# Kernel optimization log

Hardware: AMD Instinct MI355X
Metric: run time of the kernel (lower is better)

Reference implementation:

```python
import jax, jax.numpy as jnp
import numpy as np

N_HEADS = 16
EPS = 1e-5  # torch nn.LayerNorm default


def layernorm(x, g, b):
    mu = x.mean(-1, keepdims=True)
    var = ((x - mu) ** 2).mean(-1, keepdims=True)
    return (x - mu) * jax.lax.rsqrt(var + EPS) * g + b


def setup_inputs() -> dict:
    V, D, Dff, L, S, B = 32000, 1024, 4096, 6, 2048, 1
    key = jax.random.key(0)
    ks = jax.random.split(key, 12)
    std = 0.02  # GPT-2 init
    nrm = lambda k, shp: jax.random.normal(k, shp, jnp.float32) * std
    return {
        "tokens": jax.random.randint(ks[0], (B, S), 0, V),
        "tok_emb": nrm(ks[1], (V, D)),          # tied with lm head
        "pos_emb": nrm(ks[2], (S, D)),
        "Wq": nrm(ks[3], (L, D, D)), "bq": jnp.zeros((L, D)),
        "Wk": nrm(ks[4], (L, D, D)), "bk": jnp.zeros((L, D)),
        "Wv": nrm(ks[5], (L, D, D)), "bv": jnp.zeros((L, D)),
        "Wo": nrm(ks[6], (L, D, D)), "bo": jnp.zeros((L, D)),
        "ln1_g": jnp.ones((L, D)), "ln1_b": jnp.zeros((L, D)),
        "ln2_g": jnp.ones((L, D)), "ln2_b": jnp.zeros((L, D)),
        "W1": nrm(ks[7], (L, D, Dff)), "b1": jnp.zeros((L, Dff)),
        "W2": nrm(ks[8], (L, Dff, D)), "b2": jnp.zeros((L, D)),
        "lnf_g": jnp.ones((D,)), "lnf_b": jnp.zeros((D,)),
    }


def reference(tokens, tok_emb, pos_emb, Wq, bq, Wk, bk, Wv, bv, Wo, bo,
              ln1_g, ln1_b, ln2_g, ln2_b, W1, b1, W2, b2, lnf_g, lnf_b):
    B, S = tokens.shape
    D = tok_emb.shape[1]
    dk = D // N_HEADS
    scale = 1.0 / np.sqrt(dk)

    x = tok_emb[tokens] + pos_emb[:S][None]           # (B,S,D); dropout p=0 -> identity
    causal = jnp.tril(jnp.ones((S, S), bool))

    def block(x, p):
        wq, bq_, wk, bk_, wv, bv_, wo, bo_, g1, b1_, g2, b2_, w1, bf1, w2, bf2 = p
        # --- attention sublayer (pre-norm) ---
        h = layernorm(x, g1, b1_)
        q = (h @ wq + bq_).reshape(B, S, N_HEADS, dk)
        k = (h @ wk + bk_).reshape(B, S, N_HEADS, dk)
        v = (h @ wv + bv_).reshape(B, S, N_HEADS, dk)
        scores = jnp.einsum('bqhd,bkhd->bhqk', q, k) * scale
        scores = jnp.where(causal, scores, -jnp.inf)   # masked_fill(mask==0, -inf)
        attn = jax.nn.softmax(scores, axis=-1)
        ctx = jnp.einsum('bhqk,bkhd->bqhd', attn, v).reshape(B, S, D)
        x = x + ctx @ wo + bo_
        # --- FFN sublayer (pre-norm) ---
        h = layernorm(x, g2, b2_)
        x = x + jax.nn.gelu(h @ w1 + bf1, approximate=False) @ w2 + bf2
        return x, None

    x, _ = jax.lax.scan(
        block, x,
        (Wq, bq, Wk, bk, Wv, bv, Wo, bo, ln1_g, ln1_b, ln2_g, ln2_b, W1, b1, W2, b2))
    x = layernorm(x, lnf_g, lnf_b)
    logits = x @ tok_emb.T                             # tied lm head (no bias)
    return logits
```

## Files before the change

### kernel.cpp

```cpp
#include <hip/hip_runtime.h>
#include <hip/hip_bf16.h>
#include <cstdint>
#include <cstddef>


typedef __attribute__((ext_vector_type(4))) float  f32x4;
typedef __attribute__((ext_vector_type(8))) __bf16 bf16x8;
typedef __attribute__((ext_vector_type(4))) __bf16 bf16x4;

#define S_LEN 2048
#define DMODEL 1024
#define DFF 4096
#define NLAYER 6
#define NHEAD 16
#define DK 64
#define VOCAB 32000

__device__ __forceinline__ void gload_lds16(const void* g, void* l) {
    __builtin_amdgcn_global_load_lds(
        (__attribute__((address_space(1))) void*)(void*)(g),
        (__attribute__((address_space(3))) void*)(l), 16, 0, 0);
}

__global__ __launch_bounds__(256) void transpose_cvt64(
    const float* __restrict__ in, __bf16* __restrict__ out,
    int K, int N, size_t in_lstride, size_t out_lstride) {
    __shared__ float tile[64][65];
    const float* inp = in + blockIdx.z * in_lstride;
    __bf16* outp = out + blockIdx.z * out_lstride;
    const int n0 = blockIdx.x * 64, k0 = blockIdx.y * 64;
    const int t = threadIdx.x;
    const int lc = t & 15, rr = t >> 4;
#pragma unroll
    for (int i = 0; i < 4; ++i) {
        float4 v = *(const float4*)&inp[(size_t)(k0 + rr + i * 16) * N + n0 + lc * 4];
        tile[rr + i * 16][lc * 4 + 0] = v.x;
        tile[rr + i * 16][lc * 4 + 1] = v.y;
        tile[rr + i * 16][lc * 4 + 2] = v.z;
        tile[rr + i * 16][lc * 4 + 3] = v.w;
    }
    __syncthreads();
    const int a = t & 7, b = t >> 3;
#pragma unroll
    for (int j = 0; j < 2; ++j) {
        const int n = b + j * 32;
        bf16x8 o;
#pragma unroll
        for (int e = 0; e < 8; ++e) o[e] = (__bf16)tile[a * 8 + e][n];
        *(bf16x8*)&outp[(size_t)(n0 + n) * K + k0 + a * 8] = o;
    }
}

__global__ __launch_bounds__(256) void cvt_bf16(
    const float* __restrict__ in, __bf16* __restrict__ out, long n4) {
    long i = (long)blockIdx.x * 256 + threadIdx.x;
    if (i >= n4) return;
    float4 v = ((const float4*)in)[i];
    bf16x4 o = {(__bf16)v.x, (__bf16)v.y, (__bf16)v.z, (__bf16)v.w};
    ((bf16x4*)out)[i] = o;
}

__global__ __launch_bounds__(256) void embed_kernel(
    const int* __restrict__ tokens, const float* __restrict__ te,
    const float* __restrict__ pe, float* __restrict__ x) {
    const int s = blockIdx.x, t = threadIdx.x;
    const int tok = tokens[s];
    float4 a = ((const float4*)(te + (size_t)tok * DMODEL))[t];
    float4 p = ((const float4*)(pe + (size_t)s * DMODEL))[t];
    float4 r = {a.x + p.x, a.y + p.y, a.z + p.z, a.w + p.w};
    ((float4*)(x + (size_t)s * DMODEL))[t] = r;
}

__global__ __launch_bounds__(256) void ln_kernel(
    const float* __restrict__ x, const float* __restrict__ g,
    const float* __restrict__ b, __bf16* __restrict__ out) {
    const int row = blockIdx.x, t = threadIdx.x;
    float4 v = ((const float4*)(x + (size_t)row * DMODEL))[t];
    float s  = v.x + v.y + v.z + v.w;
    float s2 = v.x * v.x + v.y * v.y + v.z * v.z + v.w * v.w;
#pragma unroll
    for (int off = 1; off < 64; off <<= 1) {
        s  += __shfl_xor(s, off);
        s2 += __shfl_xor(s2, off);
    }
    __shared__ float ss[4], ss2[4];
    const int wave = t >> 6;
    if ((t & 63) == 0) { ss[wave] = s; ss2[wave] = s2; }
    __syncthreads();
    s  = ss[0] + ss[1] + ss[2] + ss[3];
    s2 = ss2[0] + ss2[1] + ss2[2] + ss2[3];
    const float mu  = s * (1.0f / DMODEL);
    const float var = s2 * (1.0f / DMODEL) - mu * mu;
    const float rstd = rsqrtf(var + 1e-5f);
    float4 gg = ((const float4*)g)[t];
    float4 bb = ((const float4*)b)[t];
    __bf16* o = out + (size_t)row * DMODEL + t * 4;
    o[0] = (__bf16)((v.x - mu) * rstd * gg.x + bb.x);
    o[1] = (__bf16)((v.y - mu) * rstd * gg.y + bb.y);
    o[2] = (__bf16)((v.z - mu) * rstd * gg.z + bb.z);
    o[3] = (__bf16)((v.w - mu) * rstd * gg.w + bb.w);
}

template <int BM, int BN, int BK, int SPLITK, int MODE, int XCD>
__global__ __launch_bounds__(256) void gemm_tiled(
    const __bf16* __restrict__ A, const __bf16* __restrict__ BT,
    int M, int N, int K,
    const float* __restrict__ bias,
    float* __restrict__ fout,
    __bf16* __restrict__ bfout,
    __bf16* __restrict__ qb, __bf16* __restrict__ kb, __bf16* __restrict__ vb,
    const float* __restrict__ bq, const float* __restrict__ bk,
    const float* __restrict__ bv) {
    constexpr int SLOTS = BK / 8;
    constexpr int SH    = (BK == 64) ? 0 : 1;
    constexpr int RPC   = 2048 / BK;
    constexpr int ACH_A = BM / RPC;
    constexpr int ACH_B = BN / RPC;
    constexpr int LOADS = ACH_A + ACH_B;
    constexpr int MR = BM / 32;
    constexpr int NR = BN / 32;
    constexpr int KS = BK / 32;
    __shared__ alignas(16) __bf16 As[2][BM * BK];
    __shared__ alignas(16) __bf16 Bs[2][BN * BK];
    const int t = threadIdx.x;
    const int wave = t >> 6, lane = t & 63;
    const int wr = wave >> 1, wc = wave & 1;
    const int lg = lane >> 4, lr = lane & 15;

    int bx = blockIdx.x, by = blockIdx.y;
    if (XCD) {
        const int nwg = gridDim.x * gridDim.y;
        const int wgid = by * gridDim.x + bx;
        const int sw = (wgid & 7) * (nwg >> 3) + (wgid >> 3);
        bx = sw % gridDim.x;
        by = sw / gridDim.x;
    }
    const int row0 = bx * BM, col0 = by * BN;
    const int kz = (SPLITK > 1) ? blockIdx.z : 0;
    const int Ksl = K / SPLITK;

    f32x4 acc[MR][NR];
#pragma unroll
    for (int i = 0; i < MR; i++)
#pragma unroll
        for (int j = 0; j < NR; j++) acc[i][j] = f32x4{0.f, 0.f, 0.f, 0.f};

    const int srow = t / SLOTS;
    const int sks = ((t % SLOTS) ^ ((srow >> SH) & (SLOTS - 1))) * 8;
    const __bf16* Ab = A + (size_t)(row0 + srow) * K + kz * Ksl + sks;
    const __bf16* Bb = BT + (size_t)(col0 + srow) * K + kz * Ksl + sks;

    const int nt = Ksl / BK;
#pragma unroll
    for (int ch = 0; ch < ACH_A; ++ch)
        gload_lds16(Ab + (size_t)ch * RPC * K, &As[0][ch * 2048 + wave * 512]);
#pragma unroll
    for (int ch = 0; ch < ACH_B; ++ch)
        gload_lds16(Bb + (size_t)ch * RPC * K, &Bs[0][ch * 2048 + wave * 512]);

    int c = 0;
    for (int T = 0; T < nt; ++T) {
        if (T + 1 < nt) {
            const int k0 = (T + 1) * BK;
#pragma unroll
            for (int ch = 0; ch < ACH_A; ++ch)
                gload_lds16(Ab + (size_t)ch * RPC * K + k0,
                            &As[c ^ 1][ch * 2048 + wave * 512]);
#pragma unroll
            for (int ch = 0; ch < ACH_B; ++ch)
                gload_lds16(Bb + (size_t)ch * RPC * K + k0,
                            &Bs[c ^ 1][ch * 2048 + wave * 512]);
            if constexpr (LOADS == 3)
                asm volatile("s_waitcnt vmcnt(3)" ::: "memory");
            else if constexpr (LOADS == 4)
                asm volatile("s_waitcnt vmcnt(4)" ::: "memory");
            else if constexpr (LOADS == 6)
                asm volatile("s_waitcnt vmcnt(6)" ::: "memory");
            else
                asm volatile("s_waitcnt vmcnt(8)" ::: "memory");
        } else {
            asm volatile("s_waitcnt vmcnt(0)" ::: "memory");
        }
        __builtin_amdgcn_s_barrier();
        asm volatile("" ::: "memory");

        bf16x8 af[MR][KS], bfr[NR][KS];
#pragma unroll
        for (int i = 0; i < MR; i++)
#pragma unroll
            for (int ks = 0; ks < KS; ks++) {
                const int row = wr * (BM / 2) + i * 16 + lr;
                const int ph = ((ks * 4 + lg) ^ ((row >> SH) & (SLOTS - 1)));
                af[i][ks] = *(const bf16x8*)&As[c][row * BK + ph * 8];
            }
#pragma unroll
        for (int j = 0; j < NR; j++)
#pragma unroll
            for (int ks = 0; ks < KS; ks++) {
                const int n = wc * (BN / 2) + j * 16 + lr;
                const int ph = ((ks * 4 + lg) ^ ((n >> SH) & (SLOTS - 1)));
                bfr[j][ks] = *(const bf16x8*)&Bs[c][n * BK + ph * 8];
            }
        __builtin_amdgcn_s_setprio(1);
#pragma unroll
        for (int i = 0; i < MR; i++)
#pragma unroll
            for (int j = 0; j < NR; j++)
#pragma unroll
                for (int ks = 0; ks < KS; ks++)
                    acc[i][j] = __builtin_amdgcn_mfma_f32_16x16x32_bf16(
                        af[i][ks], bfr[j][ks], acc[i][j], 0, 0, 0);
        __builtin_amdgcn_s_setprio(0);
        asm volatile("" ::: "memory");
        __builtin_amdgcn_s_barrier();
        c ^= 1;
    }

#pragma unroll
    for (int i = 0; i < MR; i++) {
#pragma unroll
        for (int j = 0; j < NR; j++) {
#pragma unroll
            for (int r = 0; r < 4; r++) {
                const int row = row0 + wr * (BM / 2) + i * 16 + lg * 4 + r;
                const int col = col0 + wc * (BN / 2) + j * 16 + lr;
                float v = acc[i][j][r];
                if (MODE == 0) {
                    const int sec = col >> 10, cn = col & 1023;
                    const int head = cn >> 6, d = cn & 63;
                    if (sec == 0) {
                        v = (v + bq[cn]) * 0.125f;
                        qb[((size_t)head * S_LEN + row) * DK + d] = (__bf16)v;
                    } else if (sec == 1) {
                        v = v + bk[cn];
                        kb[((size_t)head * S_LEN + row) * DK + d] = (__bf16)v;
                    } else {
                        v = v + bv[cn];
                        vb[((size_t)head * DK + d) * S_LEN + row] = (__bf16)v;
                    }
                } else if (MODE == 1) {
                    const size_t idx = (size_t)row * N + col;
                    if (SPLITK > 1) {
                        atomicAdd(&fout[idx], v + (kz == 0 ? bias[col] : 0.f));
                    } else {
                        fout[idx] = fout[idx] + v + bias[col];
                    }
                } else if (MODE == 2) {
                    const float gg = v + bias[col];
                    const float cgl = 0.5f * gg * (1.0f + erff(gg * 0.70710678118654752f));
                    bfout[(size_t)row * N + col] = (__bf16)cgl;
                } else {
                    __builtin_nontemporal_store(v, &fout[(size_t)row * N + col]);
                }
            }
        }
    }
}

__global__ __launch_bounds__(256) void attn_kernel(
    const __bf16* __restrict__ q, const __bf16* __restrict__ k,
    const __bf16* __restrict__ vt, __bf16* __restrict__ ctx) {
    const int qblk = blockIdx.x, head = blockIdx.y;
    const int t = threadIdx.x;
    const int wave = t >> 6, lane = t & 63;
    const int lg = lane >> 4, lr = lane & 15;
    const int rowbase = qblk * 64 + wave * 16;

    const __bf16* qh = q + (size_t)head * S_LEN * DK;
    const __bf16* kh = k + (size_t)head * S_LEN * DK;
    const __bf16* vh = vt + (size_t)head * DK * S_LEN;

    __shared__ alignas(16) __bf16 pls[4][16 * 72];
    __bf16* pw = pls[wave];

    bf16x8 qf0 = *(const bf16x8*)&qh[(size_t)(rowbase + lr) * DK + lg * 8];
    bf16x8 qf1 = *(const bf16x8*)&qh[(size_t)(rowbase + lr) * DK + 32 + lg * 8];

    f32x4 oacc[4];
#pragma unroll
    for (int j = 0; j < 4; j++) oacc[j] = f32x4{0.f, 0.f, 0.f, 0.f};
    float m[4], l[4];
#pragma unroll
    for (int r = 0; r < 4; r++) { m[r] = -__builtin_inff(); l[r] = 0.f; }

    for (int tt = 0; tt <= qblk; ++tt) {
        const int kv0 = tt * 64;
        f32x4 sc[4];
        __builtin_amdgcn_s_setprio(1);
#pragma unroll
        for (int jn = 0; jn < 4; jn++) {
            bf16x8 kf0 = *(const bf16x8*)&kh[(size_t)(kv0 + jn * 16 + lr) * DK + lg * 8];
            bf16x8 kf1 = *(const bf16x8*)&kh[(size_t)(kv0 + jn * 16 + lr) * DK + 32 + lg * 8];
            sc[jn] = __builtin_amdgcn_mfma_f32_16x16x32_bf16(
                qf0, kf0, f32x4{0.f, 0.f, 0.f, 0.f}, 0, 0, 0);
            sc[jn] = __builtin_amdgcn_mfma_f32_16x16x32_bf16(qf1, kf1, sc[jn], 0, 0, 0);
        }
        __builtin_amdgcn_s_setprio(0);

        if (tt == qblk) {
#pragma unroll
            for (int jn = 0; jn < 4; jn++)
#pragma unroll
                for (int r = 0; r < 4; r++) {
                    const int qrow = rowbase + lg * 4 + r;
                    if (kv0 + jn * 16 + lr > qrow) sc[jn][r] = -__builtin_inff();
                }
        }

        float mt[4];
#pragma unroll
        for (int r = 0; r < 4; r++)
            mt[r] = fmaxf(fmaxf(sc[0][r], sc[1][r]), fmaxf(sc[2][r], sc[3][r]));
#pragma unroll
        for (int off = 1; off < 16; off <<= 1)
#pragma unroll
            for (int r = 0; r < 4; r++) mt[r] = fmaxf(mt[r], __shfl_xor(mt[r], off));

        float alpha[4], psum[4];
#pragma unroll
        for (int r = 0; r < 4; r++) {
            const float mn = fmaxf(m[r], mt[r]);
            alpha[r] = __expf(m[r] - mn);
            m[r] = mn;
#pragma unroll
            for (int jn = 0; jn < 4; jn++) sc[jn][r] = __expf(sc[jn][r] - mn);
            psum[r] = (sc[0][r] + sc[1][r]) + (sc[2][r] + sc[3][r]);
        }
#pragma unroll
        for (int off = 1; off < 16; off <<= 1)
#pragma unroll
            for (int r = 0; r < 4; r++) psum[r] += __shfl_xor(psum[r], off);
#pragma unroll
        for (int r = 0; r < 4; r++) l[r] = l[r] * alpha[r] + psum[r];
#pragma unroll
        for (int j = 0; j < 4; j++)
#pragma unroll
            for (int r = 0; r < 4; r++) oacc[j][r] *= alpha[r];

#pragma unroll
        for (int r = 0; r < 4; r++)
#pragma unroll
            for (int jn = 0; jn < 4; jn++)
                pw[(lg * 4 + r) * 72 + jn * 16 + lr] = (__bf16)sc[jn][r];

        bf16x8 pf0 = *(const bf16x8*)&pw[lr * 72 + lg * 8];
        bf16x8 pf1 = *(const bf16x8*)&pw[lr * 72 + 32 + lg * 8];
        __builtin_amdgcn_s_setprio(1);
#pragma unroll
        for (int j = 0; j < 4; j++) {
            bf16x8 vf0 = *(const bf16x8*)&vh[(size_t)(j * 16 + lr) * S_LEN + kv0 + lg * 8];
            oacc[j] = __builtin_amdgcn_mfma_f32_16x16x32_bf16(pf0, vf0, oacc[j], 0, 0, 0);
            bf16x8 vf1 = *(const bf16x8*)&vh[(size_t)(j * 16 + lr) * S_LEN + kv0 + 32 + lg * 8];
            oacc[j] = __builtin_amdgcn_mfma_f32_16x16x32_bf16(pf1, vf1, oacc[j], 0, 0, 0);
        }
        __builtin_amdgcn_s_setprio(0);
    }

#pragma unroll
    for (int j = 0; j < 4; j++)
#pragma unroll
        for (int r = 0; r < 4; r++) {
            const int row = rowbase + lg * 4 + r;
            ctx[(size_t)row * DMODEL + head * DK + j * 16 + lr] =
                (__bf16)(oacc[j][r] / l[r]);
        }
}

extern "C" void kernel_launch(void* const* d_in, const int* in_sizes, int n_in,
                              void* d_out, int out_size, void* d_ws, size_t ws_size,
                              hipStream_t stream) {
    const int*   tokens  = (const int*)d_in[0];
    const float* tok_emb = (const float*)d_in[1];
    const float* pos_emb = (const float*)d_in[2];
    const float* Wq = (const float*)d_in[3];
    const float* bq = (const float*)d_in[4];
    const float* Wk = (const float*)d_in[5];
    const float* bk = (const float*)d_in[6];
    const float* Wv = (const float*)d_in[7];
    const float* bv = (const float*)d_in[8];
    const float* Wo = (const float*)d_in[9];
    const float* bo = (const float*)d_in[10];
    const float* ln1_g = (const float*)d_in[11];
    const float* ln1_b = (const float*)d_in[12];
    const float* ln2_g = (const float*)d_in[13];
    const float* ln2_b = (const float*)d_in[14];
    const float* W1 = (const float*)d_in[15];
    const float* b1 = (const float*)d_in[16];
    const float* W2 = (const float*)d_in[17];
    const float* b2 = (const float*)d_in[18];
    const float* lnf_g = (const float*)d_in[19];
    const float* lnf_b = (const float*)d_in[20];

    char* ws = (char*)d_ws;
    size_t off = 0;
    auto alloc = [&](size_t bytes) {
        char* p = ws + off;
        off = (off + bytes + 255) & ~(size_t)255;
        return p;
    };
    __bf16* wqkv_t = (__bf16*)alloc((size_t)NLAYER * 3072 * 1024 * 2);
    __bf16* wo_t   = (__bf16*)alloc((size_t)NLAYER * 1024 * 1024 * 2);
    __bf16* w1_t   = (__bf16*)alloc((size_t)NLAYER * 4096 * 1024 * 2);
    __bf16* w2_t   = (__bf16*)alloc((size_t)NLAYER * 1024 * 4096 * 2);
    __bf16* temb   = (__bf16*)alloc((size_t)VOCAB * DMODEL * 2);
    float*  x      = (float*)alloc((size_t)S_LEN * DMODEL * 4);
    __bf16* h      = (__bf16*)alloc((size_t)S_LEN * DMODEL * 2);
    __bf16* qbuf   = (__bf16*)alloc((size_t)NHEAD * S_LEN * DK * 2);
    __bf16* kbuf   = (__bf16*)alloc((size_t)NHEAD * S_LEN * DK * 2);
    __bf16* vbuf   = (__bf16*)alloc((size_t)NHEAD * S_LEN * DK * 2);
    __bf16* ctx    = (__bf16*)alloc((size_t)S_LEN * DMODEL * 2);
    __bf16* ffn    = (__bf16*)alloc((size_t)S_LEN * DFF * 2);
    if (off > ws_size) return;

    const dim3 blk256(256);

    transpose_cvt64<<<dim3(16, 16, NLAYER), blk256, 0, stream>>>(
        Wq, wqkv_t + (size_t)0 * 1024 * 1024, 1024, 1024,
        (size_t)1024 * 1024, (size_t)3072 * 1024);
    transpose_cvt64<<<dim3(16, 16, NLAYER), blk256, 0, stream>>>(
        Wk, wqkv_t + (size_t)1 * 1024 * 1024, 1024, 1024,
        (size_t)1024 * 1024, (size_t)3072 * 1024);
    transpose_cvt64<<<dim3(16, 16, NLAYER), blk256, 0, stream>>>(
        Wv, wqkv_t + (size_t)2 * 1024 * 1024, 1024, 1024,
        (size_t)1024 * 1024, (size_t)3072 * 1024);
    transpose_cvt64<<<dim3(16, 16, NLAYER), blk256, 0, stream>>>(
        Wo, wo_t, 1024, 1024, (size_t)1024 * 1024, (size_t)1024 * 1024);
    transpose_cvt64<<<dim3(64, 16, NLAYER), blk256, 0, stream>>>(
        W1, w1_t, 1024, 4096, (size_t)1024 * 4096, (size_t)4096 * 1024);
    transpose_cvt64<<<dim3(16, 64, NLAYER), blk256, 0, stream>>>(
        W2, w2_t, 4096, 1024, (size_t)4096 * 1024, (size_t)1024 * 4096);
    cvt_bf16<<<dim3((VOCAB * DMODEL / 4 + 255) / 256), blk256, 0, stream>>>(
        tok_emb, temb, (long)VOCAB * DMODEL / 4);

    embed_kernel<<<dim3(S_LEN), blk256, 0, stream>>>(tokens, tok_emb, pos_emb, x);

    for (int l = 0; l < NLAYER; ++l) {
        ln_kernel<<<dim3(S_LEN), blk256, 0, stream>>>(
            x, ln1_g + l * 1024, ln1_b + l * 1024, h);
        gemm_tiled<64, 128, 64, 1, 0, 0><<<dim3(32, 24), blk256, 0, stream>>>(
            h, wqkv_t + (size_t)l * 3072 * 1024, S_LEN, 3072, 1024,
            nullptr, nullptr, nullptr, qbuf, kbuf, vbuf,
            bq + l * 1024, bk + l * 1024, bv + l * 1024);
        attn_kernel<<<dim3(S_LEN / 64, NHEAD), blk256, 0, stream>>>(
            qbuf, kbuf, vbuf, ctx);
        gemm_tiled<64, 128, 64, 2, 1, 0><<<dim3(32, 8, 2), blk256, 0, stream>>>(
            ctx, wo_t + (size_t)l * 1024 * 1024, S_LEN, 1024, 1024,
            bo + l * 1024, x, nullptr, nullptr, nullptr, nullptr,
            nullptr, nullptr, nullptr);
        ln_kernel<<<dim3(S_LEN), blk256, 0, stream>>>(
            x, ln2_g + l * 1024, ln2_b + l * 1024, h);
        gemm_tiled<128, 128, 64, 1, 2, 0><<<dim3(16, 32), blk256, 0, stream>>>(
            h, w1_t + (size_t)l * 4096 * 1024, S_LEN, 4096, 1024,
            b1 + l * 4096, nullptr, ffn, nullptr, nullptr, nullptr,
            nullptr, nullptr, nullptr);
        gemm_tiled<64, 128, 64, 2, 1, 0><<<dim3(32, 8, 2), blk256, 0, stream>>>(
            ffn, w2_t + (size_t)l * 1024 * 4096, S_LEN, 1024, 4096,
            b2 + l * 1024, x, nullptr, nullptr, nullptr, nullptr,
            nullptr, nullptr, nullptr);
    }

    ln_kernel<<<dim3(S_LEN), blk256, 0, stream>>>(x, lnf_g, lnf_b, h);
    gemm_tiled<128, 256, 32, 1, 3, 1><<<dim3(16, 125), blk256, 0, stream>>>(
        h, temb, S_LEN, VOCAB, 1024,
        nullptr, (float*)d_out, nullptr, nullptr, nullptr, nullptr,
        nullptr, nullptr, nullptr);
}
```

Before: 1.867 ms.

## Triple-buffer GEMM loads, replace split-K atomics with partials fused into layernorm

```diff
diff --git a/kernel.cpp b/kernel.cpp
--- a/kernel.cpp
+++ b/kernel.cpp
@@ -15,6 +15,7 @@
 #define NHEAD 16
 #define DK 64
 #define VOCAB 32000
+#define MN (S_LEN * DMODEL)
 
 __device__ __forceinline__ void gload_lds16(const void* g, void* l) {
     __builtin_amdgcn_global_load_lds(
@@ -71,11 +72,22 @@
     ((float4*)(x + (size_t)s * DMODEL))[t] = r;
 }
 
+template <int NPART>
 __global__ __launch_bounds__(256) void ln_kernel(
-    const float* __restrict__ x, const float* __restrict__ g,
-    const float* __restrict__ b, __bf16* __restrict__ out) {
+    float* __restrict__ x, const float* __restrict__ p,
+    const float* __restrict__ g, const float* __restrict__ b,
+    __bf16* __restrict__ out) {
     const int row = blockIdx.x, t = threadIdx.x;
     float4 v = ((const float4*)(x + (size_t)row * DMODEL))[t];
+    if (NPART == 2) {
+        float4 a0 = ((const float4*)(p + (size_t)row * DMODEL))[t];
+        float4 a1 = ((const float4*)(p + MN + (size_t)row * DMODEL))[t];
+        v.x += a0.x + a1.x;
+        v.y += a0.y + a1.y;
+        v.z += a0.z + a1.z;
+        v.w += a0.w + a1.w;
+        ((float4*)(x + (size_t)row * DMODEL))[t] = v;
+    }
     float s  = v.x + v.y + v.z + v.w;
     float s2 = v.x * v.x + v.y * v.y + v.z * v.z + v.w * v.w;
 #pragma unroll
@@ -120,8 +132,8 @@
     constexpr int MR = BM / 32;
     constexpr int NR = BN / 32;
     constexpr int KS = BK / 32;
-    __shared__ alignas(16) __bf16 As[2][BM * BK];
-    __shared__ alignas(16) __bf16 Bs[2][BN * BK];
+    __shared__ alignas(16) __bf16 As[3][BM * BK];
+    __shared__ alignas(16) __bf16 Bs[3][BN * BK];
     const int t = threadIdx.x;
     const int wave = t >> 6, lane = t & 63;
     const int wr = wave >> 1, wc = wave & 1;
@@ -151,38 +163,36 @@
     const __bf16* Bb = BT + (size_t)(col0 + srow) * K + kz * Ksl + sks;
 
     const int nt = Ksl / BK;
-#pragma unroll
-    for (int ch = 0; ch < ACH_A; ++ch)
-        gload_lds16(Ab + (size_t)ch * RPC * K, &As[0][ch * 2048 + wave * 512]);
-#pragma unroll
-    for (int ch = 0; ch < ACH_B; ++ch)
-        gload_lds16(Bb + (size_t)ch * RPC * K, &Bs[0][ch * 2048 + wave * 512]);
-
-    int c = 0;
+    auto stage = [&](int T, int buf) {
+        const int k0 = T * BK;
+#pragma unroll
+        for (int ch = 0; ch < ACH_A; ++ch)
+            gload_lds16(Ab + (size_t)ch * RPC * K + k0,
+                        &As[buf][ch * 2048 + wave * 512]);
+#pragma unroll
+        for (int ch = 0; ch < ACH_B; ++ch)
+            gload_lds16(Bb + (size_t)ch * RPC * K + k0,
+                        &Bs[buf][ch * 2048 + wave * 512]);
+    };
+    stage(0, 0);
+    stage(1, 1);
+
+    int cc = 0, cs = 2;
     for (int T = 0; T < nt; ++T) {
         if (T + 1 < nt) {
-            const int k0 = (T + 1) * BK;
-#pragma unroll
-            for (int ch = 0; ch < ACH_A; ++ch)
-                gload_lds16(Ab + (size_t)ch * RPC * K + k0,
-                            &As[c ^ 1][ch * 2048 + wave * 512]);
-#pragma unroll
-            for (int ch = 0; ch < ACH_B; ++ch)
-                gload_lds16(Bb + (size_t)ch * RPC * K + k0,
-                            &Bs[c ^ 1][ch * 2048 + wave * 512]);
-            if constexpr (LOADS == 3)
-                asm volatile("s_waitcnt vmcnt(3)" ::: "memory");
-            else if constexpr (LOADS == 4)
+            if constexpr (LOADS == 6)
+                asm volatile("s_waitcnt vmcnt(6)" ::: "memory");
+            else if constexpr (LOADS == 8)
+                asm volatile("s_waitcnt vmcnt(8)" ::: "memory");
+            else
                 asm volatile("s_waitcnt vmcnt(4)" ::: "memory");
-            else if constexpr (LOADS == 6)
-                asm volatile("s_waitcnt vmcnt(6)" ::: "memory");
-            else
-                asm volatile("s_waitcnt vmcnt(8)" ::: "memory");
         } else {
             asm volatile("s_waitcnt vmcnt(0)" ::: "memory");
         }
         __builtin_amdgcn_s_barrier();
         asm volatile("" ::: "memory");
+
+        if (T + 2 < nt) stage(T + 2, cs);
 
         bf16x8 af[MR][KS], bfr[NR][KS];
 #pragma unroll
@@ -191,7 +201,7 @@
             for (int ks = 0; ks < KS; ks++) {
                 const int row = wr * (BM / 2) + i * 16 + lr;
                 const int ph = ((ks * 4 + lg) ^ ((row >> SH) & (SLOTS - 1)));
-                af[i][ks] = *(const bf16x8*)&As[c][row * BK + ph * 8];
+                af[i][ks] = *(const bf16x8*)&As[cc][row * BK + ph * 8];
             }
 #pragma unroll
         for (int j = 0; j < NR; j++)
@@ -199,7 +209,7 @@
             for (int ks = 0; ks < KS; ks++) {
                 const int n = wc * (BN / 2) + j * 16 + lr;
                 const int ph = ((ks * 4 + lg) ^ ((n >> SH) & (SLOTS - 1)));
-                bfr[j][ks] = *(const bf16x8*)&Bs[c][n * BK + ph * 8];
+                bfr[j][ks] = *(const bf16x8*)&Bs[cc][n * BK + ph * 8];
             }
         __builtin_amdgcn_s_setprio(1);
 #pragma unroll
@@ -211,9 +221,8 @@
                     acc[i][j] = __builtin_amdgcn_mfma_f32_16x16x32_bf16(
                         af[i][ks], bfr[j][ks], acc[i][j], 0, 0, 0);
         __builtin_amdgcn_s_setprio(0);
-        asm volatile("" ::: "memory");
-        __builtin_amdgcn_s_barrier();
-        c ^= 1;
+        cc = (cc == 2) ? 0 : cc + 1;
+        cs = (cs == 2) ? 0 : cs + 1;
     }
 
 #pragma unroll
@@ -229,7 +238,7 @@
                     const int sec = col >> 10, cn = col & 1023;
                     const int head = cn >> 6, d = cn & 63;
                     if (sec == 0) {
-                        v = (v + bq[cn]) * 0.125f;
+                        v = (v + bq[cn]) * 0.18033688011112042f;
                         qb[((size_t)head * S_LEN + row) * DK + d] = (__bf16)v;
                     } else if (sec == 1) {
                         v = v + bk[cn];
@@ -238,17 +247,14 @@
                         v = v + bv[cn];
                         vb[((size_t)head * DK + d) * S_LEN + row] = (__bf16)v;
                     }
-                } else if (MODE == 1) {
-                    const size_t idx = (size_t)row * N + col;
-                    if (SPLITK > 1) {
-                        atomicAdd(&fout[idx], v + (kz == 0 ? bias[col] : 0.f));
-                    } else {
-                        fout[idx] = fout[idx] + v + bias[col];
-                    }
                 } else if (MODE == 2) {
                     const float gg = v + bias[col];
                     const float cgl = 0.5f * gg * (1.0f + erff(gg * 0.70710678118654752f));
                     bfout[(size_t)row * N + col] = (__bf16)cgl;
+                } else if (MODE == 6) {
+                    const float vv = v + (kz == 0 ? bias[col] : 0.f);
+                    __builtin_nontemporal_store(
+                        vv, &fout[(size_t)kz * MN + (size_t)row * N + col]);
                 } else {
                     __builtin_nontemporal_store(v, &fout[(size_t)row * N + col]);
                 }
@@ -320,10 +326,10 @@
 #pragma unroll
         for (int r = 0; r < 4; r++) {
             const float mn = fmaxf(m[r], mt[r]);
-            alpha[r] = __expf(m[r] - mn);
+            alpha[r] = exp2f(m[r] - mn);
             m[r] = mn;
 #pragma unroll
-            for (int jn = 0; jn < 4; jn++) sc[jn][r] = __expf(sc[jn][r] - mn);
+            for (int jn = 0; jn < 4; jn++) sc[jn][r] = exp2f(sc[jn][r] - mn);
             psum[r] = (sc[0][r] + sc[1][r]) + (sc[2][r] + sc[3][r]);
         }
 #pragma unroll
@@ -403,14 +409,17 @@
     __bf16* w1_t   = (__bf16*)alloc((size_t)NLAYER * 4096 * 1024 * 2);
     __bf16* w2_t   = (__bf16*)alloc((size_t)NLAYER * 1024 * 4096 * 2);
     __bf16* temb   = (__bf16*)alloc((size_t)VOCAB * DMODEL * 2);
-    float*  x      = (float*)alloc((size_t)S_LEN * DMODEL * 4);
-    __bf16* h      = (__bf16*)alloc((size_t)S_LEN * DMODEL * 2);
-    __bf16* qbuf   = (__bf16*)alloc((size_t)NHEAD * S_LEN * DK * 2);
-    __bf16* kbuf   = (__bf16*)alloc((size_t)NHEAD * S_LEN * DK * 2);
-    __bf16* vbuf   = (__bf16*)alloc((size_t)NHEAD * S_LEN * DK * 2);
-    __bf16* ctx    = (__bf16*)alloc((size_t)S_LEN * DMODEL * 2);
+    float*  x      = (float*)alloc((size_t)MN * 4);
+    __bf16* h      = (__bf16*)alloc((size_t)MN * 2);
+    __bf16* qbuf   = (__bf16*)alloc((size_t)MN * 2);
+    __bf16* kbuf   = (__bf16*)alloc((size_t)MN * 2);
+    __bf16* vbuf   = (__bf16*)alloc((size_t)MN * 2);
+    __bf16* ctx    = (__bf16*)alloc((size_t)MN * 2);
     __bf16* ffn    = (__bf16*)alloc((size_t)S_LEN * DFF * 2);
     if (off > ws_size) return;
+
+    float* pproj  = (float*)ffn;
+    float* pffn2  = (float*)qbuf;
 
     const dim3 blk256(256);
 
@@ -433,33 +442,37 @@
         tok_emb, temb, (long)VOCAB * DMODEL / 4);
 
     embed_kernel<<<dim3(S_LEN), blk256, 0, stream>>>(tokens, tok_emb, pos_emb, x);
+    ln_kernel<0><<<dim3(S_LEN), blk256, 0, stream>>>(
+        x, nullptr, ln1_g, ln1_b, h);
 
     for (int l = 0; l < NLAYER; ++l) {
-        ln_kernel<<<dim3(S_LEN), blk256, 0, stream>>>(
-            x, ln1_g + l * 1024, ln1_b + l * 1024, h);
         gemm_tiled<64, 128, 64, 1, 0, 0><<<dim3(32, 24), blk256, 0, stream>>>(
             h, wqkv_t + (size_t)l * 3072 * 1024, S_LEN, 3072, 1024,
             nullptr, nullptr, nullptr, qbuf, kbuf, vbuf,
             bq + l * 1024, bk + l * 1024, bv + l * 1024);
         attn_kernel<<<dim3(S_LEN / 64, NHEAD), blk256, 0, stream>>>(
             qbuf, kbuf, vbuf, ctx);
-        gemm_tiled<64, 128, 64, 2, 1, 0><<<dim3(32, 8, 2), blk256, 0, stream>>>(
+        gemm_tiled<64, 128, 64, 2, 6, 0><<<dim3(32, 8, 2), blk256, 0, stream>>>(
             ctx, wo_t + (size_t)l * 1024 * 1024, S_LEN, 1024, 1024,
-            bo + l * 1024, x, nullptr, nullptr, nullptr, nullptr,
+            bo + l * 1024, pproj, nullptr, nullptr, nullptr, nullptr,
             nullptr, nullptr, nullptr);
-        ln_kernel<<<dim3(S_LEN), blk256, 0, stream>>>(
-            x, ln2_g + l * 1024, ln2_b + l * 1024, h);
-        gemm_tiled<128, 128, 64, 1, 2, 0><<<dim3(16, 32), blk256, 0, stream>>>(
+        ln_kernel<2><<<dim3(S_LEN), blk256, 0, stream>>>(
+            x, pproj, ln2_g + l * 1024, ln2_b + l * 1024, h);
+        gemm_tiled<64, 128, 64, 1, 2, 0><<<dim3(32, 32), blk256, 0, stream>>>(
             h, w1_t + (size_t)l * 4096 * 1024, S_LEN, 4096, 1024,
             b1 + l * 4096, nullptr, ffn, nullptr, nullptr, nullptr,
             nullptr, nullptr, nullptr);
-        gemm_tiled<64, 128, 64, 2, 1, 0><<<dim3(32, 8, 2), blk256, 0, stream>>>(
+        gemm_tiled<64, 128, 64, 2, 6, 0><<<dim3(32, 8, 2), blk256, 0, stream>>>(
             ffn, w2_t + (size_t)l * 1024 * 4096, S_LEN, 1024, 4096,
-            b2 + l * 1024, x, nullptr, nullptr, nullptr, nullptr,
+            b2 + l * 1024, pffn2, nullptr, nullptr, nullptr, nullptr,
             nullptr, nullptr, nullptr);
-    }
-
-    ln_kernel<<<dim3(S_LEN), blk256, 0, stream>>>(x, lnf_g, lnf_b, h);
+        if (l + 1 < NLAYER) {
+            ln_kernel<2><<<dim3(S_LEN), blk256, 0, stream>>>(
+                x, pffn2, ln1_g + (l + 1) * 1024, ln1_b + (l + 1) * 1024, h);
+        }
+    }
+
+    ln_kernel<2><<<dim3(S_LEN), blk256, 0, stream>>>(x, pffn2, lnf_g, lnf_b, h);
     gemm_tiled<128, 256, 32, 1, 3, 1><<<dim3(16, 125), blk256, 0, stream>>>(
         h, temb, S_LEN, VOCAB, 1024,
         nullptr, (float*)d_out, nullptr, nullptr, nullptr, nullptr,
```

After: 2.036 ms. +9.0%, slower.
